# Kernel tuning notes

Measured on AMD Instinct MI355X. Metric: run time of the kernel, lower is better.

## Reference

```python
import jax, jax.numpy as jnp
import numpy as np

SCOPE = 5
MASK_MAG = 9999.0


def setup_inputs() -> dict:
    key = jax.random.key(0)
    k1, k2, k3, k4 = jax.random.split(key, 4)
    B, T, F = 32, 2048, 256
    dataInput = jax.random.normal(k1, (B, T, F), dtype=jnp.float32)
    seqInput = jax.random.randint(k2, (B,), 1, T + 1)  # valid lengths in [1, T]
    seqInput = seqInput.at[0].set(T)  # torch code requires max(seqInput) == T
    W = jax.random.normal(k3, (SCOPE, F), dtype=jnp.float32) * 0.05  # Linear(F*scope -> 1) weight, reshaped
    b = jax.random.normal(k4, (1,), dtype=jnp.float32) * 0.05
    return {"dataInput": dataInput, "seqInput": seqInput, "W": W, "b": b,
            "hiddenNoduleNumbers": F}


def reference(dataInput, seqInput, W, b, hiddenNoduleNumbers):
    # dataInput: [B, T, F]; W: [scope, F]; b: [1]; seqInput: [B] lengths.
    B, T, F = dataInput.shape
    scope = W.shape[0]
    # Zero-pad `scope` frames at the end (torch pads scope rows then slices v:T+v).
    padded = jnp.concatenate(
        [dataInput, jnp.zeros((B, scope, F), dtype=dataInput.dtype)], axis=1)
    # Sliding-window linear score computed on-the-fly (no [B,T,scope*F] concat):
    # score[b,t] = sum_v padded[b, t+v, :] . W[v] + b
    scores = b[0] + sum(
        jnp.einsum('btf,f->bt', padded[:, v:T + v, :], W[v])
        for v in range(scope))  # [B, T]
    # AttentionMask: +9999 for valid positions, -9999 past the length; combined via min.
    valid = jnp.arange(T)[None, :] < seqInput[:, None]
    mask = jnp.where(valid, MASK_MAG, -MASK_MAG).astype(scores.dtype)
    maskedScores = jnp.minimum(scores, mask)
    attentionWeight = jax.nn.softmax(maskedScores, axis=-1)[:, :, None]  # [B, T, 1]
    attentionResult = jnp.sum(dataInput * attentionWeight, axis=1)  # [B, F]
    return attentionResult, attentionWeight
```

## Files before the change

kernel.cpp:

```cpp
#include <hip/hip_runtime.h>
#include <cfloat>

#define SCOPE 5
#define MASK_MAG 9999.0f
constexpr int F = 256;
constexpr int TW = 16;
constexpr int WAVES = 4;

template <int CTRL>
__device__ __forceinline__ float dppadd(float x) {
    int v = __builtin_amdgcn_update_dpp(0, __float_as_int(x), CTRL, 0xF, 0xF, true);
    return x + __int_as_float(v);
}
__device__ __forceinline__ float wave_sum(float s) {
    s = dppadd<0xB1>(s);
    s = dppadd<0x4E>(s);
    s = dppadd<0x141>(s);
    s = dppadd<0x140>(s);
    s += __shfl_xor(s, 16, 64);
    s += __shfl_xor(s, 32, 64);
    return s;
}

__global__ __launch_bounds__(256, 4) void fused_kernel(
    const float* __restrict__ data, const float* __restrict__ W,
    const float* __restrict__ bias, const int* __restrict__ seq,
    float* __restrict__ scores, float* __restrict__ pacc,
    float* __restrict__ pm, float* __restrict__ ps, int T) {
    const int b = blockIdx.y;
    const int tid = threadIdx.x;
    const int lane = tid & 63;
    const int wid = tid >> 6;
    const int lane4 = lane * 4;
    const int t0 = (blockIdx.x * WAVES + wid) * TW;
    const float* __restrict__ dBase = data + (size_t)b * T * F;
    float* __restrict__ sb = scores + (size_t)b * T;
    const float bv = bias[0];
    const int L = seq[b];

    float4 w[SCOPE];
    #pragma unroll
    for (int v = 0; v < SCOPE; ++v)
        w[v] = *(const float4*)(W + v * F + lane4);

    const float4 fz = make_float4(0.f, 0.f, 0.f, 0.f);
    float4 S[16];

#define LOADROW(slot, off) do { \
    const int uu = t0 + (off); \
    S[slot] = (uu < T) ? *(const float4*)(dBase + (size_t)uu * F + lane4) : fz; \
    } while (0)
#define DOT4(a, b) ((a).x*(b).x + (a).y*(b).y + (a).z*(b).z + (a).w*(b).w)

    #pragma unroll
    for (int k = 0; k < 16; ++k) LOADROW(k, k);

    float m_run = -FLT_MAX, s_run = 0.f;
    float4 acc = fz;
    float sc[8];

    #pragma unroll
    for (int j = 0; j < 8; ++j) {
        float s = DOT4(S[j], w[0]) + DOT4(S[j+1], w[1]) + DOT4(S[j+2], w[2])
                + DOT4(S[j+3], w[3]) + DOT4(S[j+4], w[4]);
        s = wave_sum(s) + bv;
        const int t = t0 + j;
        if (lane == 0) sb[t] = s;
        sc[j] = fminf(s, (t < L) ? MASK_MAG : -MASK_MAG);
    }
    {
        float gm = fmaxf(fmaxf(fmaxf(sc[0], sc[1]), fmaxf(sc[2], sc[3])),
                         fmaxf(fmaxf(sc[4], sc[5]), fmaxf(sc[6], sc[7])));
        const float m_new = fmaxf(m_run, gm);
        const float corr = expf(m_run - m_new);
        float psum = 0.f; float4 ga = fz;
        #pragma unroll
        for (int j = 0; j < 8; ++j) {
            const float p = expf(sc[j] - m_new);
            psum += p;
            ga.x += p * S[j].x; ga.y += p * S[j].y;
            ga.z += p * S[j].z; ga.w += p * S[j].w;
        }
        s_run = s_run * corr + psum;
        acc.x = acc.x * corr + ga.x; acc.y = acc.y * corr + ga.y;
        acc.z = acc.z * corr + ga.z; acc.w = acc.w * corr + ga.w;
        m_run = m_new;
    }
    #pragma unroll
    for (int k = 0; k < 4; ++k) LOADROW(k, 16 + k);

    #pragma unroll
    for (int j = 0; j < 8; ++j) {
        float s = DOT4(S[(8+j) & 15], w[0]) + DOT4(S[(9+j) & 15], w[1])
                + DOT4(S[(10+j) & 15], w[2]) + DOT4(S[(11+j) & 15], w[3])
                + DOT4(S[(12+j) & 15], w[4]);
        s = wave_sum(s) + bv;
        const int t = t0 + 8 + j;
        if (lane == 0) sb[t] = s;
        sc[j] = fminf(s, (t < L) ? MASK_MAG : -MASK_MAG);
    }
    {
        float gm = fmaxf(fmaxf(fmaxf(sc[0], sc[1]), fmaxf(sc[2], sc[3])),
                         fmaxf(fmaxf(sc[4], sc[5]), fmaxf(sc[6], sc[7])));
        const float m_new = fmaxf(m_run, gm);
        const float corr = expf(m_run - m_new);
        float psum = 0.f; float4 ga = fz;
        #pragma unroll
        for (int j = 0; j < 8; ++j) {
            const float p = expf(sc[j] - m_new);
            psum += p;
            ga.x += p * S[8 + j].x; ga.y += p * S[8 + j].y;
            ga.z += p * S[8 + j].z; ga.w += p * S[8 + j].w;
        }
        s_run = s_run * corr + psum;
        acc.x = acc.x * corr + ga.x; acc.y = acc.y * corr + ga.y;
        acc.z = acc.z * corr + ga.z; acc.w = acc.w * corr + ga.w;
        m_run = m_new;
    }
#undef DOT4
#undef LOADROW

    __shared__ float macc[WAVES][F];
    __shared__ float mm[WAVES], ss[WAVES];
    *reinterpret_cast<float4*>(&macc[wid][lane4]) = acc;
    if (lane == 0) { mm[wid] = m_run; ss[wid] = s_run; }
    __syncthreads();

    const float M = fmaxf(fmaxf(mm[0], mm[1]), fmaxf(mm[2], mm[3]));
    float e0 = expf(mm[0] - M), e1 = expf(mm[1] - M);
    float e2 = expf(mm[2] - M), e3 = expf(mm[3] - M);
    const float s_blk = e0 * ss[0] + e1 * ss[1] + e2 * ss[2] + e3 * ss[3];

    const int blk = blockIdx.x;
    const int npb = gridDim.x;
    const float ab = e0 * macc[0][tid] + e1 * macc[1][tid]
                   + e2 * macc[2][tid] + e3 * macc[3][tid];
    pacc[((size_t)(b * npb + blk)) * F + tid] = ab;
    if (tid == 0) { pm[b * npb + blk] = M; ps[b * npb + blk] = s_blk; }
}

__global__ __launch_bounds__(256) void finalize_kernel(
    const float* __restrict__ scores, const float* __restrict__ pacc,
    const float* __restrict__ pm, const float* __restrict__ ps,
    const int* __restrict__ seq, float* __restrict__ out_res,
    float* __restrict__ out_w, int T, int npb) {
    const int b = blockIdx.x;
    const int part = blockIdx.y;
    const int tid = threadIdx.x;
    __shared__ float MS[2];
    __shared__ float scale[64];

    if (tid < 64) {
        const bool v = tid < npb;
        const float m = v ? pm[b * npb + tid] : -FLT_MAX;
        const float s = v ? ps[b * npb + tid] : 0.f;
        float M = m;
        #pragma unroll
        for (int off = 32; off >= 1; off >>= 1) M = fmaxf(M, __shfl_xor(M, off, 64));
        const float e = v ? expf(m - M) : 0.f;
        float se = e * s;
        #pragma unroll
        for (int off = 32; off >= 1; off >>= 1) se += __shfl_xor(se, off, 64);
        scale[tid] = e;
        if (tid == 0) { MS[0] = M; MS[1] = 1.0f / se; }
    }
    __syncthreads();
    const float M = MS[0], invS = MS[1];

    if (part == 0) {
        float o = 0.f;
        for (int i = 0; i < npb; ++i)
            o += scale[i] * pacc[((size_t)(b * npb + i)) * F + tid];
        out_res[(size_t)b * F + tid] = o * invS;
    } else {
        const int L = seq[b];
        const int chunk = T / 8;
        const int tbase = (part - 1) * chunk;
        for (int t = tbase + tid; t < tbase + chunk; t += 256) {
            const float raw = scores[(size_t)b * T + t];
            const float msk = fminf(raw, (t < L) ? MASK_MAG : -MASK_MAG);
            out_w[(size_t)b * T + t] = expf(msk - M) * invS;
        }
    }
}

extern "C" void kernel_launch(void* const* d_in, const int* in_sizes, int n_in,
                              void* d_out, int out_size, void* d_ws, size_t ws_size,
                              hipStream_t stream) {
    const float* data = (const float*)d_in[0];
    const int*   seq  = (const int*)d_in[1];
    const float* W    = (const float*)d_in[2];
    const float* bias = (const float*)d_in[3];

    const int B  = in_sizes[1];
    const int Fr = in_sizes[2] / SCOPE;
    const int T  = in_sizes[0] / (B * Fr);
    (void)Fr;
    const int npb = T / (WAVES * TW);

    float* out_res = (float*)d_out;
    float* out_w   = (float*)d_out + (size_t)B * F;

    float* scores = (float*)d_ws;
    float* pacc   = scores + (size_t)B * T;
    float* pm     = pacc + (size_t)B * npb * F;
    float* ps     = pm + (size_t)B * npb;

    dim3 g1(npb, B);
    fused_kernel<<<g1, 256, 0, stream>>>(data, W, bias, seq, scores, pacc, pm, ps, T);
    dim3 g2(B, 9);
    finalize_kernel<<<g2, 256, 0, stream>>>(scores, pacc, pm, ps, seq, out_res, out_w, T, npb);
}
```

Measured before the change: 38.03 us.

## Double per-wave time tile and write per-wave partials, dropping block-level merge

Each wave now handles 32 timesteps with a 24-entry register ring buffer and staged prefetches, halving the 4-row halo overhead per wave and halving the block count. The in-block LDS merge and __syncthreads are removed; each wave writes its own partial max/sum/accumulator, and the finalize kernel merges 64 per-wave partials per batch. The occupancy hint in launch bounds is dropped, so register pressure rises and occupancy may fall. The finalize's bounds check on partial count is removed, which assumes exactly 64 partials (T=2048, TW=32).

```diff
diff --git a/kernel.cpp b/kernel.cpp
--- a/kernel.cpp
+++ b/kernel.cpp
@@ -4,7 +4,7 @@
 #define SCOPE 5
 #define MASK_MAG 9999.0f
 constexpr int F = 256;
-constexpr int TW = 16;
+constexpr int TW = 32;
 constexpr int WAVES = 4;
 
 template <int CTRL>
@@ -22,7 +22,7 @@
     return s;
 }
 
-__global__ __launch_bounds__(256, 4) void fused_kernel(
+__global__ __launch_bounds__(256) void fused_kernel(
     const float* __restrict__ data, const float* __restrict__ W,
     const float* __restrict__ bias, const int* __restrict__ seq,
     float* __restrict__ scores, float* __restrict__ pacc,
@@ -32,7 +32,9 @@
     const int lane = tid & 63;
     const int wid = tid >> 6;
     const int lane4 = lane * 4;
-    const int t0 = (blockIdx.x * WAVES + wid) * TW;
+    const int widx = blockIdx.x * WAVES + wid;
+    const int t0 = widx * TW;
+    const int npw = T / TW;
     const float* __restrict__ dBase = data + (size_t)b * T * F;
     float* __restrict__ sb = scores + (size_t)b * T;
     const float bv = bias[0];
@@ -44,8 +46,9 @@
         w[v] = *(const float4*)(W + v * F + lane4);
 
     const float4 fz = make_float4(0.f, 0.f, 0.f, 0.f);
-    float4 S[16];
+    float4 S[24];
 
+#define SLOT(r) ((r) % 24)
 #define LOADROW(slot, off) do { \
     const int uu = t0 + (off); \
     S[slot] = (uu < T) ? *(const float4*)(dBase + (size_t)uu * F + lane4) : fz; \
@@ -53,90 +56,61 @@
 #define DOT4(a, b) ((a).x*(b).x + (a).y*(b).y + (a).z*(b).z + (a).w*(b).w)
 
     #pragma unroll
-    for (int k = 0; k < 16; ++k) LOADROW(k, k);
+    for (int k = 0; k < 24; ++k) LOADROW(k, k);
 
     float m_run = -FLT_MAX, s_run = 0.f;
     float4 acc = fz;
     float sc[8];
 
     #pragma unroll
-    for (int j = 0; j < 8; ++j) {
-        float s = DOT4(S[j], w[0]) + DOT4(S[j+1], w[1]) + DOT4(S[j+2], w[2])
-                + DOT4(S[j+3], w[3]) + DOT4(S[j+4], w[4]);
-        s = wave_sum(s) + bv;
-        const int t = t0 + j;
-        if (lane == 0) sb[t] = s;
-        sc[j] = fminf(s, (t < L) ? MASK_MAG : -MASK_MAG);
-    }
-    {
-        float gm = fmaxf(fmaxf(fmaxf(sc[0], sc[1]), fmaxf(sc[2], sc[3])),
-                         fmaxf(fmaxf(sc[4], sc[5]), fmaxf(sc[6], sc[7])));
-        const float m_new = fmaxf(m_run, gm);
-        const float corr = expf(m_run - m_new);
-        float psum = 0.f; float4 ga = fz;
+    for (int g = 0; g < 4; ++g) {
+        const int tb = g * 8;
         #pragma unroll
         for (int j = 0; j < 8; ++j) {
-            const float p = expf(sc[j] - m_new);
-            psum += p;
-            ga.x += p * S[j].x; ga.y += p * S[j].y;
-            ga.z += p * S[j].z; ga.w += p * S[j].w;
+            float s = DOT4(S[SLOT(tb + j)],     w[0])
+                    + DOT4(S[SLOT(tb + j + 1)], w[1])
+                    + DOT4(S[SLOT(tb + j + 2)], w[2])
+                    + DOT4(S[SLOT(tb + j + 3)], w[3])
+                    + DOT4(S[SLOT(tb + j + 4)], w[4]);
+            s = wave_sum(s) + bv;
+            const int t = t0 + tb + j;
+            if (lane == 0) sb[t] = s;
+            sc[j] = fminf(s, (t < L) ? MASK_MAG : -MASK_MAG);
         }
-        s_run = s_run * corr + psum;
-        acc.x = acc.x * corr + ga.x; acc.y = acc.y * corr + ga.y;
-        acc.z = acc.z * corr + ga.z; acc.w = acc.w * corr + ga.w;
-        m_run = m_new;
-    }
-    #pragma unroll
-    for (int k = 0; k < 4; ++k) LOADROW(k, 16 + k);
-
-    #pragma unroll
-    for (int j = 0; j < 8; ++j) {
-        float s = DOT4(S[(8+j) & 15], w[0]) + DOT4(S[(9+j) & 15], w[1])
-                + DOT4(S[(10+j) & 15], w[2]) + DOT4(S[(11+j) & 15], w[3])
-                + DOT4(S[(12+j) & 15], w[4]);
-        s = wave_sum(s) + bv;
-        const int t = t0 + 8 + j;
-        if (lane == 0) sb[t] = s;
-        sc[j] = fminf(s, (t < L) ? MASK_MAG : -MASK_MAG);
-    }
-    {
-        float gm = fmaxf(fmaxf(fmaxf(sc[0], sc[1]), fmaxf(sc[2], sc[3])),
-                         fmaxf(fmaxf(sc[4], sc[5]), fmaxf(sc[6], sc[7])));
-        const float m_new = fmaxf(m_run, gm);
-        const float corr = expf(m_run - m_new);
-        float psum = 0.f; float4 ga = fz;
-        #pragma unroll
-        for (int j = 0; j < 8; ++j) {
-            const float p = expf(sc[j] - m_new);
-            psum += p;
-            ga.x += p * S[8 + j].x; ga.y += p * S[8 + j].y;
-            ga.z += p * S[8 + j].z; ga.w += p * S[8 + j].w;
+        {
+            float gm = fmaxf(fmaxf(fmaxf(sc[0], sc[1]), fmaxf(sc[2], sc[3])),
+                             fmaxf(fmaxf(sc[4], sc[5]), fmaxf(sc[6], sc[7])));
+            const float m_new = fmaxf(m_run, gm);
+            const float corr = expf(m_run - m_new);
+            float psum = 0.f; float4 ga = fz;
+            #pragma unroll
+            for (int j = 0; j < 8; ++j) {
+                const float p = expf(sc[j] - m_new);
+                psum += p;
+                const float4 r = S[SLOT(tb + j)];
+                ga.x += p * r.x; ga.y += p * r.y;
+                ga.z += p * r.z; ga.w += p * r.w;
+            }
+            s_run = s_run * corr + psum;
+            acc.x = acc.x * corr + ga.x; acc.y = acc.y * corr + ga.y;
+            acc.z = acc.z * corr + ga.z; acc.w = acc.w * corr + ga.w;
+            m_run = m_new;
         }
-        s_run = s_run * corr + psum;
-        acc.x = acc.x * corr + ga.x; acc.y = acc.y * corr + ga.y;
-        acc.z = acc.z * corr + ga.z; acc.w = acc.w * corr + ga.w;
-        m_run = m_new;
+        if (g == 0) {
+            #pragma unroll
+            for (int k = 0; k < 8; ++k) LOADROW(SLOT(24 + k), 24 + k);
+        } else if (g == 1) {
+            #pragma unroll
+            for (int k = 0; k < 4; ++k) LOADROW(SLOT(32 + k), 32 + k);
+        }
     }
 #undef DOT4
 #undef LOADROW
+#undef SLOT
 
-    __shared__ float macc[WAVES][F];
-    __shared__ float mm[WAVES], ss[WAVES];
-    *reinterpret_cast<float4*>(&macc[wid][lane4]) = acc;
-    if (lane == 0) { mm[wid] = m_run; ss[wid] = s_run; }
-    __syncthreads();
-
-    const float M = fmaxf(fmaxf(mm[0], mm[1]), fmaxf(mm[2], mm[3]));
-    float e0 = expf(mm[0] - M), e1 = expf(mm[1] - M);
-    float e2 = expf(mm[2] - M), e3 = expf(mm[3] - M);
-    const float s_blk = e0 * ss[0] + e1 * ss[1] + e2 * ss[2] + e3 * ss[3];
-
-    const int blk = blockIdx.x;
-    const int npb = gridDim.x;
-    const float ab = e0 * macc[0][tid] + e1 * macc[1][tid]
-                   + e2 * macc[2][tid] + e3 * macc[3][tid];
-    pacc[((size_t)(b * npb + blk)) * F + tid] = ab;
-    if (tid == 0) { pm[b * npb + blk] = M; ps[b * npb + blk] = s_blk; }
+    const int pw = b * npw + widx;
+    *reinterpret_cast<float4*>(pacc + (size_t)pw * F + lane4) = acc;
+    if (lane == 0) { pm[pw] = m_run; ps[pw] = s_run; }
 }
 
 __global__ __launch_bounds__(256) void finalize_kernel(
@@ -151,13 +125,12 @@
     __shared__ float scale[64];
 
     if (tid < 64) {
-        const bool v = tid < npb;
-        const float m = v ? pm[b * npb + tid] : -FLT_MAX;
-        const float s = v ? ps[b * npb + tid] : 0.f;
+        const float m = pm[b * npb + tid];
+        const float s = ps[b * npb + tid];
         float M = m;
         #pragma unroll
         for (int off = 32; off >= 1; off >>= 1) M = fmaxf(M, __shfl_xor(M, off, 64));
-        const float e = v ? expf(m - M) : 0.f;
+        const float e = expf(m - M);
         float se = e * s;
         #pragma unroll
         for (int off = 32; off >= 1; off >>= 1) se += __shfl_xor(se, off, 64);
@@ -196,18 +169,18 @@
     const int Fr = in_sizes[2] / SCOPE;
     const int T  = in_sizes[0] / (B * Fr);
     (void)Fr;
-    const int npb = T / (WAVES * TW);
+    const int npw = T / TW;
 
     float* out_res = (float*)d_out;
     float* out_w   = (float*)d_out + (size_t)B * F;
 
     float* scores = (float*)d_ws;
     float* pacc   = scores + (size_t)B * T;
-    float* pm     = pacc + (size_t)B * npb * F;
-    float* ps     = pm + (size_t)B * npb;
+    float* pm     = pacc + (size_t)B * npw * F;
+    float* ps     = pm + (size_t)B * npw;
 
-    dim3 g1(npb, B);
+    dim3 g1(T / (WAVES * TW), B);
     fused_kernel<<<g1, 256, 0, stream>>>(data, W, bias, seq, scores, pacc, pm, ps, T);
     dim3 g2(B, 9);
-    finalize_kernel<<<g2, 256, 0, stream>>>(scores, pacc, pm, ps, seq, out_res, out_w, T, npb);
+    finalize_kernel<<<g2, 256, 0, stream>>>(scores, pacc, pm, ps, seq, out_res, out_w, T, npw);
 }
```

After: 33.51 us. -11.9%, faster.
